# Performance work log

Hardware: AMD Instinct MI355X
Metric: run time of the kernel (lower is better)

## Reference

```python
import jax, jax.numpy as jnp
import numpy as np

B, L, D = 4, 1024, 1024
H = 16
DH = D // H  # 64
CACHE_LEN = 1024


def setup_inputs() -> dict:
    key = jax.random.key(0)
    ks = jax.random.split(key, 12)
    s = 1.0 / np.sqrt(D)
    return {
        "query": jax.random.normal(ks[0], (B, L, D), jnp.float32),
        "key": jax.random.normal(ks[1], (B, L, D), jnp.float32),
        "value": jax.random.normal(ks[2], (B, L, D), jnp.float32),
        "cache": jax.random.normal(ks[3], (B, H, CACHE_LEN, 2 * DH), jnp.float32),
        "Wq": jax.random.normal(ks[4], (D, D), jnp.float32) * s,
        "bq": jnp.zeros((D,), jnp.float32),
        "Wk": jax.random.normal(ks[5], (D, D), jnp.float32) * s,
        "bk": jnp.zeros((D,), jnp.float32),
        "Wv": jax.random.normal(ks[6], (D, D), jnp.float32) * s,
        "bv": jnp.zeros((D,), jnp.float32),
        "Wo": jax.random.normal(ks[7], (D, D), jnp.float32) * s,
        "bo": jnp.zeros((D,), jnp.float32),
    }


def _split_heads(x):
    # (B, L, D) -> (B, H, L, DH)
    b, l, _ = x.shape
    return x.reshape(b, l, H, DH).transpose(0, 2, 1, 3)


def reference(query, key, value, cache, Wq, bq, Wk, bk, Wv, bv, Wo, bo):
    q = _split_heads(query @ Wq.T + bq)   # (B,H,Lq,DH)
    k = _split_heads(key @ Wk.T + bk)     # (B,H,Lk,DH)
    v = _split_heads(value @ Wv.T + bv)   # (B,H,Lk,DH)

    # KV-cache concat along sequence dim
    key_cache, value_cache = jnp.split(cache, 2, axis=-1)
    k = jnp.concatenate([key_cache, k], axis=2)   # (B,H,Lc+Lk,DH)
    v = jnp.concatenate([value_cache, v], axis=2)
    new_cache = jnp.concatenate([k, v], axis=-1)  # (B,H,Lc+Lk,2*DH)

    scores = jnp.einsum("bhqd,bhkd->bhqk", q, k) / jnp.sqrt(jnp.float32(DH))
    attn = jax.nn.softmax(scores, axis=-1)        # unmasked path (mask sentinel empty)
    out = jnp.einsum("bhqk,bhkd->bhqd", attn, v)  # (B,H,Lq,DH)
    out = out.transpose(0, 2, 1, 3).reshape(query.shape[0], -1, H * DH)
    out = out @ Wo.T + bo                         # (B,Lq,D)
    return (out, new_cache)
```

## Files before the change

### kernel.cpp

```cpp
#include <hip/hip_runtime.h>
#include <hip/hip_bf16.h>
#include <stdint.h>

constexpr int Hh = 16, Ll = 1024, Dd = 1024, DHh = 64, CL = 1024, TKV = 2048;
constexpr size_t OUT_ELEMS = 4ull * 1024 * 1024;
constexpr float LOG2E = 1.44269504088896340736f;

typedef __attribute__((ext_vector_type(8))) short short8;
typedef __attribute__((ext_vector_type(4))) float floatx4;

#define MFMA16(a, b, c) __builtin_amdgcn_mfma_f32_16x16x32_bf16(a, b, c, 0, 0, 0)

__device__ __forceinline__ float fexp2(float x) {
#if __has_builtin(__builtin_amdgcn_exp2f)
    return __builtin_amdgcn_exp2f(x);
#else
    float r;
    asm("v_exp_f32 %0, %1" : "=v"(r) : "v"(x));
    return r;
#endif
}

__device__ __forceinline__ short bfs(float x) {
    union { __hip_bfloat16 h; short s; } u;
    u.h = __float2bfloat16(x);
    return u.s;
}

__device__ __forceinline__ short8 cvt8(const float* p) {
    float4 a = *(const float4*)p;
    float4 b = *(const float4*)(p + 4);
    short8 r;
    r[0] = bfs(a.x); r[1] = bfs(a.y); r[2] = bfs(a.z); r[3] = bfs(a.w);
    r[4] = bfs(b.x); r[5] = bfs(b.y); r[6] = bfs(b.z); r[7] = bfs(b.w);
    return r;
}

__device__ __forceinline__ void gload_lds16(const __hip_bfloat16* g, __hip_bfloat16* l) {
    __builtin_amdgcn_global_load_lds((const __attribute__((address_space(1))) void*)g,
                                     (__attribute__((address_space(3))) void*)l, 16, 0, 0);
}

__device__ __forceinline__ int vswz(int d) { return ((d >> 3) ^ d) & 7; }

__global__ __launch_bounds__(256) void convert_w_kernel(
    const float* __restrict__ Wq, const float* __restrict__ Wk,
    const float* __restrict__ Wv, const float* __restrict__ Wo,
    __hip_bfloat16* __restrict__ Wb) {
    int c = blockIdx.x * 256 + threadIdx.x;
    int wsel = c >> 17;
    int within = c & 131071;
    int row = within >> 7;
    int cir = within & 127;
    int kb = cir >> 3, cw = cir & 7;
    int swc = cw ^ (row & 7);
    const float* src = (wsel == 0) ? Wq : (wsel == 1) ? Wk : (wsel == 2) ? Wv : Wo;
    *(short8*)(Wb + ((size_t)wsel << 20) + ((size_t)row << 10) + (kb << 6) + (swc << 3)) =
        cvt8(src + (size_t)within * 8);
}

__global__ __launch_bounds__(256) void gemm_qkv(
    const float* __restrict__ Aq, const float* __restrict__ Ak,
    const float* __restrict__ Av, const float* __restrict__ cache,
    const __hip_bfloat16* __restrict__ Wb,
    const float* __restrict__ bq, const float* __restrict__ bk,
    const float* __restrict__ bv, __hip_bfloat16* __restrict__ qws,
    float* __restrict__ outc, __hip_bfloat16* __restrict__ kbf,
    __hip_bfloat16* __restrict__ vbf) {
    constexpr int K = 1024, BK = 64;
    __shared__ alignas(16) __hip_bfloat16 As[64 * BK];
    __shared__ alignas(16) __hip_bfloat16 Bs[128 * BK];

    if (blockIdx.z == 0) {
        int id = blockIdx.y * 64 + blockIdx.x;
#pragma unroll
        for (int it = 0; it < 8; it++) {
            int c = id * 2048 + it * 256 + threadIdx.x;
            int bh  = c >> 14;
            int rem = c & 16383;
            int t = rem >> 4, part = rem & 15;
            const float* s = cache + (size_t)c * 8;
            float* d = outc + OUT_ELEMS + (size_t)bh * 262144 + (size_t)rem * 8;
            *(float4*)d       = *(const float4*)s;
            *(float4*)(d + 4) = *(const float4*)(s + 4);
            short8 bv8 = cvt8(s);
            if (part < 8) {
                *(short8*)&kbf[(size_t)bh * 131072 + (size_t)t * 64 +
                               ((part ^ (t & 7)) << 3)] = bv8;
            } else {
                int d0 = (part - 8) * 8;
#pragma unroll
                for (int e = 0; e < 8; e++) {
                    int dd = d0 + e;
                    ((short*)vbf)[((size_t)(bh * 16 + (t >> 7)) * 64 + dd) * 128 +
                                  ((t & 127) ^ (vswz(dd) << 3))] = bv8[e];
                }
            }
        }
        return;
    }

    const int mode = blockIdx.z - 1;
    const float* A = (mode == 0) ? Aq : (mode == 1) ? Ak : Av;
    const float* bias = (mode == 0) ? bq : (mode == 1) ? bk : bv;
    const __hip_bfloat16* W = Wb + ((size_t)mode << 20);

    const int tid = threadIdx.x;
    const int w = tid >> 6, lane = tid & 63;
    const int g = lane >> 4, lr = lane & 15;
    const int tm = blockIdx.x * 64, tn = blockIdx.y * 128;
    const int wr = (w >> 1) * 32, wc = (w & 1) * 64;

    floatx4 acc[2][4] = {};

    for (int k0 = 0; k0 < K; k0 += BK) {
        __syncthreads();
#pragma unroll
        for (int it = 0; it < 4; it++) {
            int c0 = it * 256 + w * 64;
            int c = c0 + lane;
            int row = c >> 3, col = (c & 7) * 8;
            gload_lds16(W + (size_t)(tn + row) * K + k0 + col, &Bs[c0 * 8]);
        }
#pragma unroll
        for (int it = 0; it < 2; it++) {
            int c = it * 256 + tid;
            int row = c >> 3, cw = c & 7;
            *(short8*)&As[(row * 8 + (cw ^ (row & 7))) * 8] =
                cvt8(A + (size_t)(tm + row) * K + k0 + cw * 8);
        }
        __syncthreads();
#pragma unroll
        for (int kk = 0; kk < 2; kk++) {
            short8 af[2], bf[4];
#pragma unroll
            for (int i = 0; i < 2; i++) {
                int ra = wr + i * 16 + lr;
                af[i] = *(const short8*)&As[ra * BK + (((kk * 4 + g) ^ (ra & 7)) << 3)];
            }
#pragma unroll
            for (int j = 0; j < 4; j++) {
                int rb_ = wc + j * 16 + lr;
                bf[j] = *(const short8*)&Bs[rb_ * BK + (((kk * 4 + g) ^ (rb_ & 7)) << 3)];
            }
#pragma unroll
            for (int i = 0; i < 2; i++)
#pragma unroll
                for (int j = 0; j < 4; j++)
                    acc[i][j] = MFMA16(af[i], bf[j], acc[i][j]);
        }
    }

#pragma unroll
    for (int j = 0; j < 4; j++) {
        int n = tn + wc + j * 16 + lr;
        float bv_ = bias[n];
#pragma unroll
        for (int i = 0; i < 2; i++) {
#pragma unroll
            for (int r = 0; r < 4; r++) {
                int m = tm + wr + i * 16 + g * 4 + r;
                float v = acc[i][j][r] + bv_;
                if (mode == 0) {
                    size_t addr = (size_t)(m >> 10) * ((size_t)Hh * Ll * DHh) +
                                  (size_t)(n >> 6) * ((size_t)Ll * DHh) +
                                  (size_t)(m & 1023) * DHh + (n & 63);
                    qws[addr] = __float2bfloat16(v * (0.125f * LOG2E));
                } else {
                    size_t bh = (size_t)((m >> 10) * Hh + (n >> 6));
                    size_t addr = OUT_ELEMS + (bh * TKV + CL + (m & 1023)) * 128 + (n & 63) +
                                  (mode == 2 ? 64 : 0);
                    outc[addr] = v;
                    int t = CL + (m & 1023);
                    int dd = n & 63;
                    __hip_bfloat16 hv = __float2bfloat16(v);
                    if (mode == 1) {
                        kbf[bh * 131072 + (size_t)t * 64 +
                            (((dd >> 3) ^ (t & 7)) << 3) + (dd & 7)] = hv;
                    } else {
                        vbf[(bh * 16 + (size_t)(t >> 7)) * 8192 + (size_t)dd * 128 +
                            ((t & 127) ^ (vswz(dd) << 3))] = hv;
                    }
                }
            }
        }
    }
}

__global__ __launch_bounds__(256) void gemm_out(
    const __hip_bfloat16* __restrict__ A, const __hip_bfloat16* __restrict__ W,
    const float* __restrict__ bias, float* __restrict__ C) {
    constexpr int K = 1024, BK = 64;
    __shared__ alignas(16) __hip_bfloat16 As[64 * BK];
    __shared__ alignas(16) __hip_bfloat16 Bs[128 * BK];

    const int tid = threadIdx.x;
    const int w = tid >> 6, lane = tid & 63;
    const int g = lane >> 4, lr = lane & 15;
    const int tm = blockIdx.x * 64, tn = blockIdx.y * 128;
    const int wr = (w >> 1) * 32, wc = (w & 1) * 64;

    floatx4 acc[2][4] = {};

    for (int k0 = 0; k0 < K; k0 += BK) {
        __syncthreads();
#pragma unroll
        for (int it = 0; it < 4; it++) {
            int c0 = it * 256 + w * 64;
            int c = c0 + lane;
            int row = c >> 3, col = (c & 7) * 8;
            gload_lds16(W + (size_t)(tn + row) * K + k0 + col, &Bs[c0 * 8]);
        }
#pragma unroll
        for (int it = 0; it < 2; it++) {
            int c0 = it * 256 + w * 64;
            int c = c0 + lane;
            int row = c >> 3, col = (c & 7) * 8;
            gload_lds16(A + (size_t)(tm + row) * K + k0 + col, &As[c0 * 8]);
        }
        __syncthreads();
#pragma unroll
        for (int kk = 0; kk < 2; kk++) {
            short8 af[2], bf[4];
#pragma unroll
            for (int i = 0; i < 2; i++) {
                int ra = wr + i * 16 + lr;
                af[i] = *(const short8*)&As[ra * BK + (((kk * 4 + g) ^ (ra & 7)) << 3)];
            }
#pragma unroll
            for (int j = 0; j < 4; j++) {
                int rb_ = wc + j * 16 + lr;
                bf[j] = *(const short8*)&Bs[rb_ * BK + (((kk * 4 + g) ^ (rb_ & 7)) << 3)];
            }
#pragma unroll
            for (int i = 0; i < 2; i++)
#pragma unroll
                for (int j = 0; j < 4; j++)
                    acc[i][j] = MFMA16(af[i], bf[j], acc[i][j]);
        }
    }

#pragma unroll
    for (int j = 0; j < 4; j++) {
        int n = tn + wc + j * 16 + lr;
        float bv = bias[n];
#pragma unroll
        for (int i = 0; i < 2; i++)
#pragma unroll
            for (int r = 0; r < 4; r++) {
                int m = tm + wr + i * 16 + g * 4 + r;
                C[(size_t)m * 1024 + n] = acc[i][j][r] + bv;
            }
    }
}

__global__ __launch_bounds__(512) void attn_kernel(
    const __hip_bfloat16* __restrict__ qws, const __hip_bfloat16* __restrict__ kbf,
    const __hip_bfloat16* __restrict__ vbf, __hip_bfloat16* __restrict__ ows) {
    constexpr int KVB = 128;
    __shared__ alignas(16) __hip_bfloat16 Ks[2][KVB * 64];
    __shared__ alignas(16) __hip_bfloat16 Vt[2][64 * KVB];
    __shared__ alignas(16) __hip_bfloat16 Ps[8][32 * 136];

    const int tid = threadIdx.x;
    const int w = tid >> 6, lane = tid & 63;
    const int g = lane >> 4, lr = lane & 15;
    const int bh = blockIdx.x;
    const int q0 = blockIdx.y * 256 + w * 32;

    const __hip_bfloat16* qbase = qws + (size_t)bh * Ll * DHh;
    const __hip_bfloat16* kb = kbf + (size_t)bh * 131072;
    const __hip_bfloat16* vb = vbf + (size_t)bh * 131072;

    short8 qf[2][2];
#pragma unroll
    for (int i = 0; i < 2; i++)
#pragma unroll
        for (int kk = 0; kk < 2; kk++)
            qf[i][kk] = *(const short8*)
                (qbase + (size_t)(q0 + i * 16 + lr) * DHh + kk * 32 + g * 8);

#define STAGE(b, tl)                                                          \
    {                                                                         \
        const __hip_bfloat16* kt = kb + (size_t)(tl) * 8192;                  \
        const __hip_bfloat16* vt = vb + (size_t)(tl) * 8192;                  \
        _Pragma("unroll")                                                     \
        for (int it = 0; it < 2; it++) {                                      \
            int c0 = it * 512 + w * 64;                                       \
            gload_lds16(kt + (size_t)(c0 + lane) * 8, &Ks[b][c0 * 8]);        \
            gload_lds16(vt + (size_t)(c0 + lane) * 8, &Vt[b][c0 * 8]);        \
        }                                                                     \
    }

    float rm[2][4], rl[2][4];
    floatx4 o[2][4] = {};
#pragma unroll
    for (int i = 0; i < 2; i++)
#pragma unroll
        for (int j = 0; j < 4; j++) { rm[i][j] = -3e38f; rl[i][j] = 0.f; }

    STAGE(0, 0);
    __syncthreads();

    int cur = 0;
    for (int tl = 0; tl < 16; ++tl) {
        if (tl < 15) STAGE(cur ^ 1, tl + 1);

        floatx4 s[2][8] = {};
#pragma unroll
        for (int f = 0; f < 8; f++) {
            int row = f * 16 + lr;
#pragma unroll
            for (int kk = 0; kk < 2; kk++) {
                short8 bfr = *(const short8*)
                    &Ks[cur][row * 64 + (((kk * 4 + g) ^ (row & 7)) << 3)];
                s[0][f] = MFMA16(qf[0][kk], bfr, s[0][f]);
                s[1][f] = MFMA16(qf[1][kk], bfr, s[1][f]);
            }
        }

        bool ok = true;
        float mt[2][4];
#pragma unroll
        for (int i = 0; i < 2; i++)
#pragma unroll
            for (int j = 0; j < 4; j++) {
                float mv = fmaxf(
                    fmaxf(fmaxf(s[i][0][j], s[i][1][j]), fmaxf(s[i][2][j], s[i][3][j])),
                    fmaxf(fmaxf(s[i][4][j], s[i][5][j]), fmaxf(s[i][6][j], s[i][7][j])));
                mv = fmaxf(mv, __shfl_xor(mv, 1));
                mv = fmaxf(mv, __shfl_xor(mv, 2));
                mv = fmaxf(mv, __shfl_xor(mv, 4));
                mv = fmaxf(mv, __shfl_xor(mv, 8));
                mt[i][j] = mv;
                ok = ok && (mv - rm[i][j] <= 8.f);
            }
        if (!__all(ok)) {
#pragma unroll
            for (int i = 0; i < 2; i++)
#pragma unroll
                for (int j = 0; j < 4; j++) {
                    float mn = fmaxf(rm[i][j], mt[i][j]);
                    float corr = fexp2(rm[i][j] - mn);
                    rm[i][j] = mn;
                    rl[i][j] *= corr;
#pragma unroll
                    for (int f2 = 0; f2 < 4; f2++) o[i][f2][j] = o[i][f2][j] * corr;
                }
        }
#pragma unroll
        for (int i = 0; i < 2; i++) {
            float rs[4] = {0.f, 0.f, 0.f, 0.f};
#pragma unroll
            for (int f = 0; f < 8; f++)
#pragma unroll
                for (int j = 0; j < 4; j++) {
                    float p = fexp2(s[i][f][j] - rm[i][j]);
                    s[i][f][j] = p;
                    rs[j] += p;
                }
#pragma unroll
            for (int j = 0; j < 4; j++) {
                rs[j] += __shfl_xor(rs[j], 1);
                rs[j] += __shfl_xor(rs[j], 2);
                rs[j] += __shfl_xor(rs[j], 4);
                rs[j] += __shfl_xor(rs[j], 8);
                rl[i][j] += rs[j];
            }
        }

        __hip_bfloat16* pw = &Ps[w][0];
#pragma unroll
        for (int i = 0; i < 2; i++)
#pragma unroll
            for (int f = 0; f < 8; f++)
#pragma unroll
                for (int j = 0; j < 4; j++)
                    pw[(i * 16 + g * 4 + j) * 136 + f * 16 + lr] =
                        __float2bfloat16(s[i][f][j]);

#pragma unroll
        for (int kk = 0; kk < 4; kk++) {
            short8 pa0 = *(const short8*)&pw[(0 + lr) * 136 + kk * 32 + g * 8];
            short8 pa1 = *(const short8*)&pw[(16 + lr) * 136 + kk * 32 + g * 8];
#pragma unroll
            for (int f2 = 0; f2 < 4; f2++) {
                int d = f2 * 16 + lr;
                short8 vbr = *(const short8*)
                    &Vt[cur][d * KVB + ((kk * 32 + g * 8) ^ (vswz(d) << 3))];
                o[0][f2] = MFMA16(pa0, vbr, o[0][f2]);
                o[1][f2] = MFMA16(pa1, vbr, o[1][f2]);
            }
        }

        __syncthreads();
        cur ^= 1;
    }
#undef STAGE

    const int b = bh >> 4, h = bh & 15;
#pragma unroll
    for (int i = 0; i < 2; i++)
#pragma unroll
        for (int j = 0; j < 4; j++) {
            float inv = 1.0f / rl[i][j];
            int qrow = q0 + i * 16 + g * 4 + j;
            int sr = qrow & 7;
            size_t rb = ((size_t)b * Ll + qrow) * Dd + (size_t)h * DHh;
#pragma unroll
            for (int f2 = 0; f2 < 4; f2++) {
                int ch = f2 * 2 + (lr >> 3);
                ows[rb + ((ch ^ sr) << 3) + (lr & 7)] =
                    __float2bfloat16(o[i][f2][j] * inv);
            }
        }
}

extern "C" void kernel_launch(void* const* d_in, const int* in_sizes, int n_in,
                              void* d_out, int out_size, void* d_ws, size_t ws_size,
                              hipStream_t stream) {
    (void)in_sizes; (void)n_in; (void)out_size; (void)ws_size;
    const float* query = (const float*)d_in[0];
    const float* key   = (const float*)d_in[1];
    const float* value = (const float*)d_in[2];
    const float* cache = (const float*)d_in[3];
    const float* Wq = (const float*)d_in[4];
    const float* bq = (const float*)d_in[5];
    const float* Wk = (const float*)d_in[6];
    const float* bk = (const float*)d_in[7];
    const float* Wv = (const float*)d_in[8];
    const float* bv = (const float*)d_in[9];
    const float* Wo = (const float*)d_in[10];
    const float* bo = (const float*)d_in[11];

    float* out = (float*)d_out;
    __hip_bfloat16* qws = (__hip_bfloat16*)d_ws;
    __hip_bfloat16* aws = qws + OUT_ELEMS;
    __hip_bfloat16* Wb  = aws + OUT_ELEMS;
    __hip_bfloat16* kbf = Wb  + OUT_ELEMS;
    __hip_bfloat16* vbf = kbf + (8ull << 20);

    dim3 bb(256);
    convert_w_kernel<<<dim3(2048), bb, 0, stream>>>(Wq, Wk, Wv, Wo, Wb);

    gemm_qkv<<<dim3(64, 8, 4), bb, 0, stream>>>(query, key, value, cache, Wb,
                                                bq, bk, bv, qws, out, kbf, vbf);

    attn_kernel<<<dim3(64, 4), dim3(512), 0, stream>>>(qws, kbf, vbf, aws);

    gemm_out<<<dim3(64, 8), bb, 0, stream>>>(aws, Wb + (3u << 20), bo, out);
}
```

Before: 168.0 us.

## Double-buffer shared-memory tiles in QKV projection GEMM

The QKV GEMM now keeps two LDS buffers for the A and B tiles. It issues the loads for the next K-step before running the MFMAs on the current buffer, with one barrier per iteration instead of two. This aims to overlap global-memory latency and the fp32-to-bf16 conversion with matrix math. The cost is twice the shared memory, which may lower occupancy, and the A-tile conversion still stalls on its global loads before it writes to LDS.

Result: no change. 168.8 us (+0.5%).

```diff
diff --git a/kernel.cpp b/kernel.cpp
--- a/kernel.cpp
+++ b/kernel.cpp
@@ -68,8 +68,8 @@
     float* __restrict__ outc, __hip_bfloat16* __restrict__ kbf,
     __hip_bfloat16* __restrict__ vbf) {
     constexpr int K = 1024, BK = 64;
-    __shared__ alignas(16) __hip_bfloat16 As[64 * BK];
-    __shared__ alignas(16) __hip_bfloat16 Bs[128 * BK];
+    __shared__ alignas(16) __hip_bfloat16 As[2][64 * BK];
+    __shared__ alignas(16) __hip_bfloat16 Bs[2][128 * BK];
 
     if (blockIdx.z == 0) {
         int id = blockIdx.y * 64 + blockIdx.x;
@@ -113,35 +113,43 @@
 
     floatx4 acc[2][4] = {};
 
+#define QSTAGE(b, k0)                                                         \
+    {                                                                         \
+        _Pragma("unroll")                                                     \
+        for (int it = 0; it < 4; it++) {                                      \
+            int c0 = it * 256 + w * 64;                                       \
+            int c = c0 + lane;                                                \
+            int row = c >> 3, col = (c & 7) * 8;                              \
+            gload_lds16(W + (size_t)(tn + row) * K + (k0) + col,              \
+                        &Bs[b][c0 * 8]);                                      \
+        }                                                                     \
+        _Pragma("unroll")                                                     \
+        for (int it = 0; it < 2; it++) {                                      \
+            int c = it * 256 + tid;                                           \
+            int row = c >> 3, cw = c & 7;                                     \
+            *(short8*)&As[b][(row * 8 + (cw ^ (row & 7))) * 8] =              \
+                cvt8(A + (size_t)(tm + row) * K + (k0) + cw * 8);             \
+        }                                                                     \
+    }
+
+    QSTAGE(0, 0);
+    __syncthreads();
+
+    int cur = 0;
     for (int k0 = 0; k0 < K; k0 += BK) {
-        __syncthreads();
-#pragma unroll
-        for (int it = 0; it < 4; it++) {
-            int c0 = it * 256 + w * 64;
-            int c = c0 + lane;
-            int row = c >> 3, col = (c & 7) * 8;
-            gload_lds16(W + (size_t)(tn + row) * K + k0 + col, &Bs[c0 * 8]);
-        }
-#pragma unroll
-        for (int it = 0; it < 2; it++) {
-            int c = it * 256 + tid;
-            int row = c >> 3, cw = c & 7;
-            *(short8*)&As[(row * 8 + (cw ^ (row & 7))) * 8] =
-                cvt8(A + (size_t)(tm + row) * K + k0 + cw * 8);
-        }
-        __syncthreads();
+        if (k0 + BK < K) QSTAGE(cur ^ 1, k0 + BK);
 #pragma unroll
         for (int kk = 0; kk < 2; kk++) {
             short8 af[2], bf[4];
 #pragma unroll
             for (int i = 0; i < 2; i++) {
                 int ra = wr + i * 16 + lr;
-                af[i] = *(const short8*)&As[ra * BK + (((kk * 4 + g) ^ (ra & 7)) << 3)];
+                af[i] = *(const short8*)&As[cur][ra * BK + (((kk * 4 + g) ^ (ra & 7)) << 3)];
             }
 #pragma unroll
             for (int j = 0; j < 4; j++) {
                 int rb_ = wc + j * 16 + lr;
-                bf[j] = *(const short8*)&Bs[rb_ * BK + (((kk * 4 + g) ^ (rb_ & 7)) << 3)];
+                bf[j] = *(const short8*)&Bs[cur][rb_ * BK + (((kk * 4 + g) ^ (rb_ & 7)) << 3)];
             }
 #pragma unroll
             for (int i = 0; i < 2; i++)
@@ -149,7 +157,10 @@
                 for (int j = 0; j < 4; j++)
                     acc[i][j] = MFMA16(af[i], bf[j], acc[i][j]);
         }
-    }
+        __syncthreads();
+        cur ^= 1;
+    }
+#undef QSTAGE
 
 #pragma unroll
     for (int j = 0; j < 4; j++) {
```
